# Optimization experiments

Measured on AMD Instinct MI355X. Metric: run time of the kernel, lower is better.

The kernel has to match this reference:

```python
import jax, jax.numpy as jnp
import numpy as np
import math

B, S, D_MODEL, H = 2, 2048, 1024, 16
D_HEAD = D_MODEL // H
THETA = 10000.0


def _init_linear(key, out_f, in_f):
    std = math.sqrt(2.0 / (out_f + in_f))
    w = jax.random.truncated_normal(key, -3.0, 3.0, (out_f, in_f), dtype=jnp.float32)
    return w * std


def setup_inputs() -> dict:
    key = jax.random.key(0)
    k1, k2, k3 = jax.random.split(key, 3)
    x = jax.random.normal(k1, (B, S, D_MODEL), dtype=jnp.float32)
    wqkv = _init_linear(k2, 3 * D_MODEL, D_MODEL)
    w_out = _init_linear(k3, D_MODEL, D_MODEL)
    # RoPE tables: positions [max_seq_len,1] * inv_freq [d_head//2]
    positions = jnp.arange(S, dtype=jnp.float32)[:, None]
    freqs = jnp.arange(0, D_HEAD, 2, dtype=jnp.float32) / D_HEAD
    inv_freq = 1.0 / (THETA ** freqs)
    angles = positions * inv_freq  # [S, D_HEAD//2]
    cos = jnp.cos(angles)
    sin = jnp.sin(angles)
    token_positions = jnp.arange(S, dtype=jnp.int32)
    return {"x": x, "wqkv": wqkv, "w_out": w_out, "cos": cos, "sin": sin,
            "token_positions": token_positions}


def _apply_rope(t, cos_pos, sin_pos):
    # t: [b, h, s, d], cos/sin_pos: [s, d//2] broadcast over b,h
    te = t[..., 0::2]
    to = t[..., 1::2]
    re = te * cos_pos - to * sin_pos
    ro = te * sin_pos + to * cos_pos
    # interleave even/odd back: [..., d//2, 2] -> [..., d]
    out = jnp.stack([re, ro], axis=-1)
    return out.reshape(t.shape)


def reference(x, wqkv, w_out, cos, sin, token_positions):
    b, s, d_model = x.shape
    qkv = jnp.einsum('oi,bsi->bso', wqkv, x)  # [b, s, 3*d_model]
    q, k, v = jnp.split(qkv, 3, axis=-1)

    def to_heads(t):
        return t.reshape(b, s, H, D_HEAD).transpose(0, 2, 1, 3)  # b h s d

    q, k, v = to_heads(q), to_heads(k), to_heads(v)

    cos_pos = cos[token_positions]  # [s, d_head//2]
    sin_pos = sin[token_positions]
    q = _apply_rope(q, cos_pos, sin_pos)
    k = _apply_rope(k, cos_pos, sin_pos)

    scores = jnp.einsum('bhqd,bhkd->bhqk', q, k) / math.sqrt(D_HEAD)
    causal = jnp.tril(jnp.ones((s, s), dtype=bool))  # ~triu(diag=1)
    scores = jnp.where(causal, scores, -jnp.inf)
    weights = jax.nn.softmax(scores, axis=-1)
    y = jnp.einsum('bhqk,bhkd->bhqd', weights, v)
    y = y.transpose(0, 2, 1, 3).reshape(b, s, d_model)
    return jnp.einsum('oi,bsi->bso', w_out, y)
```

## Files before the change

### kernel.cpp

```cpp
#include <hip/hip_runtime.h>
#include <hip/hip_bf16.h>


#define S_LEN 2048
#define DMODEL 1024
#define NH 16
#define QKVN 3072

typedef __attribute__((ext_vector_type(4))) short short4v;
typedef __attribute__((ext_vector_type(8))) short short8v;
typedef __attribute__((ext_vector_type(4))) float floatx4;

#define CSOFT 0.18033688f

__device__ __forceinline__ unsigned short f2bf(float f) {
  unsigned int u = __float_as_uint(f);
  u += 0x7FFFu + ((u >> 16) & 1u);
  return (unsigned short)(u >> 16);
}
__device__ __forceinline__ float bf2f(unsigned short u) {
  return __uint_as_float(((unsigned int)u) << 16);
}
__device__ __forceinline__ void gload16(const void* g, void* l) {
  __builtin_amdgcn_global_load_lds((const __attribute__((address_space(1))) void*)g,
                                   (__attribute__((address_space(3))) void*)l,
                                   16, 0, 0);
}

__global__ __launch_bounds__(256) void cast_bf16_perm_k(const float* __restrict__ in,
                                                        unsigned short* __restrict__ out,
                                                        int nchunk) {
  int i = blockIdx.x * 256 + threadIdx.x;
  if (i >= nchunk) return;
  int c = i & 3;
  const float4* f4 = reinterpret_cast<const float4*>(in);
  float4 lo = f4[(i >> 2) * 8 + c];
  float4 hi = f4[(i >> 2) * 8 + 4 + c];
  short8v o;
  o[0] = (short)f2bf(lo.x); o[1] = (short)f2bf(lo.y);
  o[2] = (short)f2bf(lo.z); o[3] = (short)f2bf(lo.w);
  o[4] = (short)f2bf(hi.x); o[5] = (short)f2bf(hi.y);
  o[6] = (short)f2bf(hi.z); o[7] = (short)f2bf(hi.w);
  reinterpret_cast<short8v*>(out)[i] = o;
}

template <bool OUT_BF16>
__global__ __launch_bounds__(256) void gemm_bt(const unsigned short* __restrict__ A,
                                               const unsigned short* __restrict__ Bm,
                                               void* __restrict__ Cp, int M, int N, int K) {
  __shared__ __align__(16) unsigned short As[128 * 32];
  __shared__ __align__(16) unsigned short Bs[128 * 32];
  const int tid = threadIdx.x;
  const int lane = tid & 63;
  const int w = tid >> 6;
  const int wm = w >> 1, wn = w & 1;
  const int l15 = lane & 15, l4 = lane >> 4;
  const int bm = blockIdx.y * 128, bn = blockIdx.x * 128;
  const int srow = lane >> 2;
  const int skc = (lane & 3) * 8;

  floatx4 acc[4][4] = {};

  for (int k0 = 0; k0 < K; k0 += 32) {
#pragma unroll
    for (int j = 0; j < 2; ++j) {
      const unsigned short* ga = A + (size_t)(bm + j * 64 + w * 16 + srow) * K + k0 + skc;
      gload16(ga, &As[j * 2048 + w * 512]);
      const unsigned short* gb = Bm + (size_t)(bn + j * 64 + w * 16 + srow) * K + k0 + skc;
      gload16(gb, &Bs[j * 2048 + w * 512]);
    }
    asm volatile("s_waitcnt vmcnt(0)" ::: "memory");
    __syncthreads();

    short8v af[4], bfr[4];
#pragma unroll
    for (int f = 0; f < 4; ++f) {
      af[f]  = *(const short8v*)(As + (wm * 64 + f * 16 + l15) * 32 + l4 * 8);
      bfr[f] = *(const short8v*)(Bs + (wn * 64 + f * 16 + l15) * 32 + l4 * 8);
    }
#pragma unroll
    for (int f = 0; f < 4; ++f)
#pragma unroll
      for (int g = 0; g < 4; ++g)
        acc[f][g] = __builtin_amdgcn_mfma_f32_16x16x32_bf16(af[f], bfr[g], acc[f][g], 0, 0, 0);
    __syncthreads();
  }

#pragma unroll
  for (int f = 0; f < 4; ++f)
#pragma unroll
    for (int g = 0; g < 4; ++g)
#pragma unroll
      for (int r = 0; r < 4; ++r) {
        int row = bm + wm * 64 + f * 16 + l4 * 4 + r;
        int col = bn + wn * 64 + g * 16 + l15;
        if (OUT_BF16)
          ((unsigned short*)Cp)[(size_t)row * N + col] = f2bf(acc[f][g][r]);
        else
          ((float*)Cp)[(size_t)row * N + col] = acc[f][g][r];
      }
}

__global__ __launch_bounds__(256) void rope_pack_k(const unsigned short* __restrict__ qkvb,
                                                   unsigned short* __restrict__ qp_,
                                                   unsigned short* __restrict__ kp_,
                                                   unsigned short* __restrict__ vtp_,
                                                   const float* __restrict__ cosp,
                                                   const float* __restrict__ sinp,
                                                   const int* __restrict__ tpos) {
  __shared__ unsigned short Vs[64][68];
  const int tid = threadIdx.x;
  const int bh = blockIdx.x >> 5;
  const int st = blockIdx.x & 31;
  const int b = bh >> 4, h = bh & 15;
  const int c = tid & 15, t0 = tid >> 4;
  const int s0 = st * 64;

#pragma unroll
  for (int it = 0; it < 4; ++it) {
    const int tl = it * 16 + t0;
    const int s = s0 + tl;
    const int tp = tpos[s];
    const size_t base = ((size_t)(b * S_LEN + s)) * QKVN + h * 64 + c * 4;
    const float co0 = cosp[tp * 32 + 2 * c], si0 = sinp[tp * 32 + 2 * c];
    const float co1 = cosp[tp * 32 + 2 * c + 1], si1 = sinp[tp * 32 + 2 * c + 1];
    {
      const float c0 = co0 * CSOFT, s0q = si0 * CSOFT;
      const float c1 = co1 * CSOFT, s1q = si1 * CSOFT;
      ushort4 rv = *(const ushort4*)(qkvb + base);
      float a0 = bf2f(rv.x), a1 = bf2f(rv.y), a2 = bf2f(rv.z), a3 = bf2f(rv.w);
      ushort4 ov;
      ov.x = f2bf(a0 * c0 - a1 * s0q); ov.y = f2bf(a0 * s0q + a1 * c0);
      ov.z = f2bf(a2 * c1 - a3 * s1q); ov.w = f2bf(a2 * s1q + a3 * c1);
      *(ushort4*)(qp_ + ((size_t)bh * S_LEN + s) * 64 + c * 4) = ov;
    }
    {
      ushort4 rv = *(const ushort4*)(qkvb + base + DMODEL);
      float a0 = bf2f(rv.x), a1 = bf2f(rv.y), a2 = bf2f(rv.z), a3 = bf2f(rv.w);
      ushort4 ov;
      ov.x = f2bf(a0 * co0 - a1 * si0); ov.y = f2bf(a0 * si0 + a1 * co0);
      ov.z = f2bf(a2 * co1 - a3 * si1); ov.w = f2bf(a2 * si1 + a3 * co1);
      *(ushort4*)(kp_ + ((size_t)bh * S_LEN + s) * 64 + c * 4) = ov;
    }
    {
      ushort4 rv = *(const ushort4*)(qkvb + base + 2 * DMODEL);
      *(ushort4*)(&Vs[tl][c * 4]) = rv;
    }
  }
  __syncthreads();
#pragma unroll
  for (int it = 0; it < 4; ++it) {
    const int d = it * 16 + t0;
    ushort4 ov;
    ov.x = Vs[c * 4 + 0][d]; ov.y = Vs[c * 4 + 1][d];
    ov.z = Vs[c * 4 + 2][d]; ov.w = Vs[c * 4 + 3][d];
    *(ushort4*)(vtp_ + ((size_t)bh * 64 + d) * S_LEN + s0 + c * 4) = ov;
  }
}

__device__ __forceinline__ short8v readfrag(const unsigned short* L, int row, int c2, int l4) {
  const int sw = row & 7;
  const int cl = c2 * 4 + (l4 >> 1);
  const int base = row * 64 + (l4 & 1) * 4;
  union { short4v h[2]; short8v v; } u;
  u.h[0] = *(const short4v*)(L + base + ((cl ^ sw) << 3));
  u.h[1] = *(const short4v*)(L + base + (((cl + 2) ^ sw) << 3));
  return u.v;
}

__device__ __forceinline__ void stage_tiles(const unsigned short* kg0, const unsigned short* vg0,
                                            int kt, unsigned short* Kb, unsigned short* Vb,
                                            int tid, int w) {
#pragma unroll
  for (int i = 0; i < 2; ++i) {
    int jj = i * 256 + tid;
    int row = jj >> 3;
    int cc = (jj & 7) ^ (row & 7);
    gload16(kg0 + (size_t)kt * 4096 + row * 64 + cc * 8, Kb + (i * 256 + w * 64) * 8);
    gload16(vg0 + (size_t)row * S_LEN + kt * 64 + cc * 8, Vb + (i * 256 + w * 64) * 8);
  }
}

__global__ __launch_bounds__(256) void attn_mfma(const unsigned short* __restrict__ qp_,
                                                 const unsigned short* __restrict__ kp_,
                                                 const unsigned short* __restrict__ vtp_,
                                                 unsigned short* __restrict__ yb) {
  __shared__ __align__(16) unsigned short Kl[2][4096];
  __shared__ __align__(16) unsigned short Vl[2][4096];
  const int tid = threadIdx.x;
  const int lane = tid & 63, w = tid >> 6;
  const int l15 = lane & 15, l4 = lane >> 4;
  const int j = blockIdx.x;
  const int bh = (j & 7) + 8 * (j >> 7);
  const int pair = (j >> 3) & 15;
  const int b = bh >> 4, h = bh & 15;

  const unsigned short* kg0 = kp_ + (size_t)bh * S_LEN * 64;
  const unsigned short* vg0 = vtp_ + (size_t)bh * 64 * S_LEN;

  for (int pass = 0; pass < 2; ++pass) {
    const int qt = pass ? pair : 31 - pair;
    const unsigned short* qp = qp_ + ((size_t)bh * S_LEN + qt * 64 + w * 16 + l15) * 64;
    short8v qf[2];
#pragma unroll
    for (int c2 = 0; c2 < 2; ++c2) {
      union { short4v h[2]; short8v v; } u;
      u.h[0] = *(const short4v*)(qp + c2 * 32 + 4 * l4);
      u.h[1] = *(const short4v*)(qp + c2 * 32 + 16 + 4 * l4);
      qf[c2] = u.v;
    }
    floatx4 o[4] = {};
    float mrun = -1e30f, lsum = 0.f;

    stage_tiles(kg0, vg0, 0, Kl[0], Vl[0], tid, w);

    for (int kt = 0; kt <= qt; ++kt) {
      const int cur = kt & 1;
      if (kt < qt) {
        stage_tiles(kg0, vg0, kt + 1, Kl[cur ^ 1], Vl[cur ^ 1], tid, w);
        asm volatile("s_waitcnt vmcnt(4)" ::: "memory");
      } else {
        asm volatile("s_waitcnt vmcnt(0)" ::: "memory");
      }
      __syncthreads();

      const unsigned short* Kc = Kl[cur];
      const unsigned short* Vc = Vl[cur];
      const bool diag = (kt == qt);
      float s_[4][4];
      __builtin_amdgcn_s_setprio(1);
#pragma unroll
      for (int g = 0; g < 4; ++g) {
        if (diag && g > w) {
          s_[g][0] = s_[g][1] = s_[g][2] = s_[g][3] = -INFINITY;
          continue;
        }
        short8v k0 = readfrag(Kc, g * 16 + l15, 0, l4);
        short8v k1 = readfrag(Kc, g * 16 + l15, 1, l4);
        floatx4 t = {0.f, 0.f, 0.f, 0.f};
        t = __builtin_amdgcn_mfma_f32_16x16x32_bf16(k0, qf[0], t, 0, 0, 0);
        t = __builtin_amdgcn_mfma_f32_16x16x32_bf16(k1, qf[1], t, 0, 0, 0);
#pragma unroll
        for (int r = 0; r < 4; ++r) {
          float v = t[r];
          if (diag && g == w && (l4 * 4 + r > l15)) v = -INFINITY;
          s_[g][r] = v;
        }
      }
      __builtin_amdgcn_s_setprio(0);

      float tm = -INFINITY;
#pragma unroll
      for (int g = 0; g < 4; ++g)
#pragma unroll
        for (int r = 0; r < 4; ++r) tm = fmaxf(tm, s_[g][r]);
      tm = fmaxf(tm, __shfl_xor(tm, 16));
      tm = fmaxf(tm, __shfl_xor(tm, 32));

      if (!__all(tm <= mrun + 3.0f)) {
        float nm = fmaxf(mrun, tm);
        float rs = exp2f(mrun - nm);
        mrun = nm;
        lsum *= rs;
        float rsr[4];
#pragma unroll
        for (int r = 0; r < 4; ++r) rsr[r] = __shfl(rs, l4 * 4 + r);
#pragma unroll
        for (int dt = 0; dt < 4; ++dt)
#pragma unroll
          for (int r = 0; r < 4; ++r) o[dt][r] *= rsr[r];
      }

      union { unsigned short u[16]; short8v v[2]; } pk;
      float psum = 0.f;
#pragma unroll
      for (int g = 0; g < 4; ++g)
#pragma unroll
        for (int r = 0; r < 4; ++r) {
          float p = exp2f(s_[g][r] - mrun);
          psum += p;
          pk.u[g * 4 + r] = f2bf(p);
        }
      lsum += psum;

      __builtin_amdgcn_s_setprio(1);
#pragma unroll
      for (int dt = 0; dt < 4; ++dt) {
        short8v v0 = readfrag(Vc, dt * 16 + l15, 0, l4);
        short8v v1 = readfrag(Vc, dt * 16 + l15, 1, l4);
        o[dt] = __builtin_amdgcn_mfma_f32_16x16x32_bf16(pk.v[0], v0, o[dt], 0, 0, 0);
        o[dt] = __builtin_amdgcn_mfma_f32_16x16x32_bf16(pk.v[1], v1, o[dt], 0, 0, 0);
      }
      __builtin_amdgcn_s_setprio(0);
      __syncthreads();
    }

    lsum += __shfl_xor(lsum, 16);
    lsum += __shfl_xor(lsum, 32);
    float linv = 1.f / lsum;
    float lr[4];
#pragma unroll
    for (int r = 0; r < 4; ++r) lr[r] = __shfl(linv, l4 * 4 + r);
#pragma unroll
    for (int dt = 0; dt < 4; ++dt)
#pragma unroll
      for (int r = 0; r < 4; ++r) {
        size_t row = (size_t)(b * S_LEN + qt * 64 + w * 16 + l4 * 4 + r);
        int col = (h * 2 + (dt >> 1)) * 32 + (l15 >> 2) * 8 + (l15 & 3) + 4 * (dt & 1);
        yb[row * DMODEL + col] = f2bf(o[dt][r] * lr[r]);
      }
  }
}

extern "C" void kernel_launch(void* const* d_in, const int* in_sizes, int n_in,
                              void* d_out, int out_size, void* d_ws, size_t ws_size,
                              hipStream_t stream) {
  const float* x     = (const float*)d_in[0];
  const float* wqkv  = (const float*)d_in[1];
  const float* w_out = (const float*)d_in[2];
  const float* cosp  = (const float*)d_in[3];
  const float* sinp  = (const float*)d_in[4];
  const int*   tpos  = (const int*)d_in[5];
  float* out = (float*)d_out;
  char* ws = (char*)d_ws;

  const size_t MB = 1024 * 1024;
  unsigned short* xb    = (unsigned short*)(ws + 0);
  unsigned short* wqkvb = (unsigned short*)(ws + 8 * MB);
  unsigned short* wob   = (unsigned short*)(ws + 14 * MB);
  unsigned short* qkvb  = (unsigned short*)(ws + 16 * MB);
  unsigned short* qpk   = (unsigned short*)(ws + 40 * MB);
  unsigned short* kpk   = (unsigned short*)(ws + 48 * MB);
  unsigned short* vtpk  = (unsigned short*)(ws + 56 * MB);
  unsigned short* yb    = (unsigned short*)(ws + 0);

  cast_bf16_perm_k<<<2048, 256, 0, stream>>>(x, xb, 524288);
  cast_bf16_perm_k<<<1536, 256, 0, stream>>>(wqkv, wqkvb, 393216);
  cast_bf16_perm_k<<<512, 256, 0, stream>>>(w_out, wob, 131072);

  gemm_bt<true><<<dim3(24, 32), 256, 0, stream>>>(xb, wqkvb, qkvb, 4096, QKVN, 1024);

  rope_pack_k<<<1024, 256, 0, stream>>>(qkvb, qpk, kpk, vtpk, cosp, sinp, tpos);

  attn_mfma<<<512, 256, 0, stream>>>(qpk, kpk, vtpk, yb);

  gemm_bt<false><<<dim3(8, 32), 256, 0, stream>>>(yb, wob, out, 4096, DMODEL, 1024);
}
```

Before: 221.8 us.

## Permute Q/K/V packing for 128-bit LDS reads, swizzle GEMM LDS, one q-tile per block

The rope pack kernel now writes Q, K and V^T with a permuted column order. This lets attention load each MFMA fragment with one 128-bit LDS read instead of two 64-bit reads, and load Q fragments directly. The GEMM rotates its 16-byte chunk placement in LDS to reduce bank conflicts. Attention no longer pairs a long and a short q-tile in one block: it launches 1024 blocks with one q-tile each, longest tiles first, which relies on the hardware scheduler to balance the causal work instead of the explicit pairing.

```diff
diff --git a/kernel.cpp b/kernel.cpp
--- a/kernel.cpp
+++ b/kernel.cpp
@@ -25,6 +25,9 @@
   __builtin_amdgcn_global_load_lds((const __attribute__((address_space(1))) void*)g,
                                    (__attribute__((address_space(3))) void*)l,
                                    16, 0, 0);
+}
+__device__ __forceinline__ int perm4(int c) {
+  return (c >> 3) * 32 + (c & 3) * 8 + ((c >> 2) & 1) * 4;
 }
 
 __global__ __launch_bounds__(256) void cast_bf16_perm_k(const float* __restrict__ in,
@@ -57,16 +60,17 @@
   const int l15 = lane & 15, l4 = lane >> 4;
   const int bm = blockIdx.y * 128, bn = blockIdx.x * 128;
   const int srow = lane >> 2;
-  const int skc = (lane & 3) * 8;
+  const int schunk = ((lane & 3) - ((lane >> 3) & 3)) & 3;
+  const int rslot = (l4 + (l15 >> 1)) & 3;
 
   floatx4 acc[4][4] = {};
 
   for (int k0 = 0; k0 < K; k0 += 32) {
 #pragma unroll
     for (int j = 0; j < 2; ++j) {
-      const unsigned short* ga = A + (size_t)(bm + j * 64 + w * 16 + srow) * K + k0 + skc;
+      const unsigned short* ga = A + (size_t)(bm + j * 64 + w * 16 + srow) * K + k0 + schunk * 8;
       gload16(ga, &As[j * 2048 + w * 512]);
-      const unsigned short* gb = Bm + (size_t)(bn + j * 64 + w * 16 + srow) * K + k0 + skc;
+      const unsigned short* gb = Bm + (size_t)(bn + j * 64 + w * 16 + srow) * K + k0 + schunk * 8;
       gload16(gb, &Bs[j * 2048 + w * 512]);
     }
     asm volatile("s_waitcnt vmcnt(0)" ::: "memory");
@@ -75,8 +79,8 @@
     short8v af[4], bfr[4];
 #pragma unroll
     for (int f = 0; f < 4; ++f) {
-      af[f]  = *(const short8v*)(As + (wm * 64 + f * 16 + l15) * 32 + l4 * 8);
-      bfr[f] = *(const short8v*)(Bs + (wn * 64 + f * 16 + l15) * 32 + l4 * 8);
+      af[f]  = *(const short8v*)(As + (wm * 64 + f * 16 + l15) * 32 + rslot * 8);
+      bfr[f] = *(const short8v*)(Bs + (wn * 64 + f * 16 + l15) * 32 + rslot * 8);
     }
 #pragma unroll
     for (int f = 0; f < 4; ++f)
@@ -115,6 +119,7 @@
   const int b = bh >> 4, h = bh & 15;
   const int c = tid & 15, t0 = tid >> 4;
   const int s0 = st * 64;
+  const int pc = perm4(c);
 
 #pragma unroll
   for (int it = 0; it < 4; ++it) {
@@ -132,7 +137,7 @@
       ushort4 ov;
       ov.x = f2bf(a0 * c0 - a1 * s0q); ov.y = f2bf(a0 * s0q + a1 * c0);
       ov.z = f2bf(a2 * c1 - a3 * s1q); ov.w = f2bf(a2 * s1q + a3 * c1);
-      *(ushort4*)(qp_ + ((size_t)bh * S_LEN + s) * 64 + c * 4) = ov;
+      *(ushort4*)(qp_ + ((size_t)bh * S_LEN + s) * 64 + pc) = ov;
     }
     {
       ushort4 rv = *(const ushort4*)(qkvb + base + DMODEL);
@@ -140,7 +145,7 @@
       ushort4 ov;
       ov.x = f2bf(a0 * co0 - a1 * si0); ov.y = f2bf(a0 * si0 + a1 * co0);
       ov.z = f2bf(a2 * co1 - a3 * si1); ov.w = f2bf(a2 * si1 + a3 * co1);
-      *(ushort4*)(kp_ + ((size_t)bh * S_LEN + s) * 64 + c * 4) = ov;
+      *(ushort4*)(kp_ + ((size_t)bh * S_LEN + s) * 64 + pc) = ov;
     }
     {
       ushort4 rv = *(const ushort4*)(qkvb + base + 2 * DMODEL);
@@ -154,18 +159,12 @@
     ushort4 ov;
     ov.x = Vs[c * 4 + 0][d]; ov.y = Vs[c * 4 + 1][d];
     ov.z = Vs[c * 4 + 2][d]; ov.w = Vs[c * 4 + 3][d];
-    *(ushort4*)(vtp_ + ((size_t)bh * 64 + d) * S_LEN + s0 + c * 4) = ov;
-  }
-}
-
-__device__ __forceinline__ short8v readfrag(const unsigned short* L, int row, int c2, int l4) {
-  const int sw = row & 7;
-  const int cl = c2 * 4 + (l4 >> 1);
-  const int base = row * 64 + (l4 & 1) * 4;
-  union { short4v h[2]; short8v v; } u;
-  u.h[0] = *(const short4v*)(L + base + ((cl ^ sw) << 3));
-  u.h[1] = *(const short4v*)(L + base + (((cl + 2) ^ sw) << 3));
-  return u.v;
+    *(ushort4*)(vtp_ + ((size_t)bh * 64 + d) * S_LEN + s0 + pc) = ov;
+  }
+}
+
+__device__ __forceinline__ short8v readfrag128(const unsigned short* L, int row, int cc) {
+  return *(const short8v*)(L + row * 64 + (((cc) ^ (row & 7)) << 3));
 }
 
 __device__ __forceinline__ void stage_tiles(const unsigned short* kg0, const unsigned short* vg0,
@@ -191,125 +190,119 @@
   const int lane = tid & 63, w = tid >> 6;
   const int l15 = lane & 15, l4 = lane >> 4;
   const int j = blockIdx.x;
-  const int bh = (j & 7) + 8 * (j >> 7);
-  const int pair = (j >> 3) & 15;
+  const int bh = (j & 7) + 8 * ((j >> 3) & 3);
+  const int qt = 31 - (j >> 5);
   const int b = bh >> 4, h = bh & 15;
 
   const unsigned short* kg0 = kp_ + (size_t)bh * S_LEN * 64;
   const unsigned short* vg0 = vtp_ + (size_t)bh * 64 * S_LEN;
 
-  for (int pass = 0; pass < 2; ++pass) {
-    const int qt = pass ? pair : 31 - pair;
-    const unsigned short* qp = qp_ + ((size_t)bh * S_LEN + qt * 64 + w * 16 + l15) * 64;
-    short8v qf[2];
-#pragma unroll
-    for (int c2 = 0; c2 < 2; ++c2) {
-      union { short4v h[2]; short8v v; } u;
-      u.h[0] = *(const short4v*)(qp + c2 * 32 + 4 * l4);
-      u.h[1] = *(const short4v*)(qp + c2 * 32 + 16 + 4 * l4);
-      qf[c2] = u.v;
-    }
-    floatx4 o[4] = {};
-    float mrun = -1e30f, lsum = 0.f;
-
-    stage_tiles(kg0, vg0, 0, Kl[0], Vl[0], tid, w);
-
-    for (int kt = 0; kt <= qt; ++kt) {
-      const int cur = kt & 1;
-      if (kt < qt) {
-        stage_tiles(kg0, vg0, kt + 1, Kl[cur ^ 1], Vl[cur ^ 1], tid, w);
-        asm volatile("s_waitcnt vmcnt(4)" ::: "memory");
-      } else {
-        asm volatile("s_waitcnt vmcnt(0)" ::: "memory");
+  const unsigned short* qp = qp_ + ((size_t)bh * S_LEN + qt * 64 + w * 16 + l15) * 64;
+  short8v qf[2];
+#pragma unroll
+  for (int c2 = 0; c2 < 2; ++c2)
+    qf[c2] = *(const short8v*)(qp + c2 * 32 + l4 * 8);
+
+  floatx4 o[4] = {};
+  float mrun = -1e30f, lsum = 0.f;
+
+  stage_tiles(kg0, vg0, 0, Kl[0], Vl[0], tid, w);
+
+  for (int kt = 0; kt <= qt; ++kt) {
+    const int cur = kt & 1;
+    if (kt < qt) {
+      stage_tiles(kg0, vg0, kt + 1, Kl[cur ^ 1], Vl[cur ^ 1], tid, w);
+      asm volatile("s_waitcnt vmcnt(4)" ::: "memory");
+    } else {
+      asm volatile("s_waitcnt vmcnt(0)" ::: "memory");
+    }
+    __syncthreads();
+
+    const unsigned short* Kc = Kl[cur];
+    const unsigned short* Vc = Vl[cur];
+    const bool diag = (kt == qt);
+    float s_[4][4];
+    __builtin_amdgcn_s_setprio(1);
+#pragma unroll
+    for (int g = 0; g < 4; ++g) {
+      if (diag && g > w) {
+        s_[g][0] = s_[g][1] = s_[g][2] = s_[g][3] = -INFINITY;
+        continue;
       }
-      __syncthreads();
-
-      const unsigned short* Kc = Kl[cur];
-      const unsigned short* Vc = Vl[cur];
-      const bool diag = (kt == qt);
-      float s_[4][4];
-      __builtin_amdgcn_s_setprio(1);
-#pragma unroll
-      for (int g = 0; g < 4; ++g) {
-        if (diag && g > w) {
-          s_[g][0] = s_[g][1] = s_[g][2] = s_[g][3] = -INFINITY;
-          continue;
-        }
-        short8v k0 = readfrag(Kc, g * 16 + l15, 0, l4);
-        short8v k1 = readfrag(Kc, g * 16 + l15, 1, l4);
-        floatx4 t = {0.f, 0.f, 0.f, 0.f};
-        t = __builtin_amdgcn_mfma_f32_16x16x32_bf16(k0, qf[0], t, 0, 0, 0);
-        t = __builtin_amdgcn_mfma_f32_16x16x32_bf16(k1, qf[1], t, 0, 0, 0);
-#pragma unroll
-        for (int r = 0; r < 4; ++r) {
-          float v = t[r];
-          if (diag && g == w && (l4 * 4 + r > l15)) v = -INFINITY;
-          s_[g][r] = v;
-        }
+      short8v k0 = readfrag128(Kc, g * 16 + l15, l4);
+      short8v k1 = readfrag128(Kc, g * 16 + l15, 4 + l4);
+      floatx4 t = {0.f, 0.f, 0.f, 0.f};
+      t = __builtin_amdgcn_mfma_f32_16x16x32_bf16(k0, qf[0], t, 0, 0, 0);
+      t = __builtin_amdgcn_mfma_f32_16x16x32_bf16(k1, qf[1], t, 0, 0, 0);
+#pragma unroll
+      for (int r = 0; r < 4; ++r) {
+        float v = t[r];
+        if (diag && g == w && (l4 * 4 + r > l15)) v = -INFINITY;
+        s_[g][r] = v;
       }
-      __builtin_amdgcn_s_setprio(0);
-
-      float tm = -INFINITY;
-#pragma unroll
-      for (int g = 0; g < 4; ++g)
-#pragma unroll
-        for (int r = 0; r < 4; ++r) tm = fmaxf(tm, s_[g][r]);
-      tm = fmaxf(tm, __shfl_xor(tm, 16));
-      tm = fmaxf(tm, __shfl_xor(tm, 32));
-
-      if (!__all(tm <= mrun + 3.0f)) {
-        float nm = fmaxf(mrun, tm);
-        float rs = exp2f(mrun - nm);
-        mrun = nm;
-        lsum *= rs;
-        float rsr[4];
-#pragma unroll
-        for (int r = 0; r < 4; ++r) rsr[r] = __shfl(rs, l4 * 4 + r);
-#pragma unroll
-        for (int dt = 0; dt < 4; ++dt)
-#pragma unroll
-          for (int r = 0; r < 4; ++r) o[dt][r] *= rsr[r];
+    }
+    __builtin_amdgcn_s_setprio(0);
+
+    float tm = -INFINITY;
+#pragma unroll
+    for (int g = 0; g < 4; ++g)
+#pragma unroll
+      for (int r = 0; r < 4; ++r) tm = fmaxf(tm, s_[g][r]);
+    tm = fmaxf(tm, __shfl_xor(tm, 16));
+    tm = fmaxf(tm, __shfl_xor(tm, 32));
+
+    if (!__all(tm <= mrun + 3.0f)) {
+      float nm = fmaxf(mrun, tm);
+      float rs = exp2f(mrun - nm);
+      mrun = nm;
+      lsum *= rs;
+      float rsr[4];
+#pragma unroll
+      for (int r = 0; r < 4; ++r) rsr[r] = __shfl(rs, l4 * 4 + r);
+#pragma unroll
+      for (int dt = 0; dt < 4; ++dt)
+#pragma unroll
+        for (int r = 0; r < 4; ++r) o[dt][r] *= rsr[r];
+    }
+
+    union { unsigned short u[16]; short8v v[2]; } pk;
+    float psum = 0.f;
+#pragma unroll
+    for (int g = 0; g < 4; ++g)
+#pragma unroll
+      for (int r = 0; r < 4; ++r) {
+        float p = exp2f(s_[g][r] - mrun);
+        psum += p;
+        pk.u[g * 4 + r] = f2bf(p);
       }
-
-      union { unsigned short u[16]; short8v v[2]; } pk;
-      float psum = 0.f;
-#pragma unroll
-      for (int g = 0; g < 4; ++g)
-#pragma unroll
-        for (int r = 0; r < 4; ++r) {
-          float p = exp2f(s_[g][r] - mrun);
-          psum += p;
-          pk.u[g * 4 + r] = f2bf(p);
-        }
-      lsum += psum;
-
-      __builtin_amdgcn_s_setprio(1);
-#pragma unroll
-      for (int dt = 0; dt < 4; ++dt) {
-        short8v v0 = readfrag(Vc, dt * 16 + l15, 0, l4);
-        short8v v1 = readfrag(Vc, dt * 16 + l15, 1, l4);
-        o[dt] = __builtin_amdgcn_mfma_f32_16x16x32_bf16(pk.v[0], v0, o[dt], 0, 0, 0);
-        o[dt] = __builtin_amdgcn_mfma_f32_16x16x32_bf16(pk.v[1], v1, o[dt], 0, 0, 0);
-      }
-      __builtin_amdgcn_s_setprio(0);
-      __syncthreads();
-    }
-
-    lsum += __shfl_xor(lsum, 16);
-    lsum += __shfl_xor(lsum, 32);
-    float linv = 1.f / lsum;
-    float lr[4];
-#pragma unroll
-    for (int r = 0; r < 4; ++r) lr[r] = __shfl(linv, l4 * 4 + r);
-#pragma unroll
-    for (int dt = 0; dt < 4; ++dt)
-#pragma unroll
-      for (int r = 0; r < 4; ++r) {
-        size_t row = (size_t)(b * S_LEN + qt * 64 + w * 16 + l4 * 4 + r);
-        int col = (h * 2 + (dt >> 1)) * 32 + (l15 >> 2) * 8 + (l15 & 3) + 4 * (dt & 1);
-        yb[row * DMODEL + col] = f2bf(o[dt][r] * lr[r]);
-      }
-  }
+    lsum += psum;
+
+    __builtin_amdgcn_s_setprio(1);
+#pragma unroll
+    for (int dt = 0; dt < 4; ++dt) {
+      short8v v0 = readfrag128(Vc, dt * 16 + l15, l4);
+      short8v v1 = readfrag128(Vc, dt * 16 + l15, 4 + l4);
+      o[dt] = __builtin_amdgcn_mfma_f32_16x16x32_bf16(pk.v[0], v0, o[dt], 0, 0, 0);
+      o[dt] = __builtin_amdgcn_mfma_f32_16x16x32_bf16(pk.v[1], v1, o[dt], 0, 0, 0);
+    }
+    __builtin_amdgcn_s_setprio(0);
+    __syncthreads();
+  }
+
+  lsum += __shfl_xor(lsum, 16);
+  lsum += __shfl_xor(lsum, 32);
+  float linv = 1.f / lsum;
+  float lr[4];
+#pragma unroll
+  for (int r = 0; r < 4; ++r) lr[r] = __shfl(linv, l4 * 4 + r);
+#pragma unroll
+  for (int dt = 0; dt < 4; ++dt)
+#pragma unroll
+    for (int r = 0; r < 4; ++r) {
+      size_t row = (size_t)(b * S_LEN + qt * 64 + w * 16 + l4 * 4 + r);
+      int col = (h * 2 + (dt >> 1)) * 32 + (l15 >> 2) * 8 + (l15 & 3) + 4 * (dt & 1);
+      yb[row * DMODEL + col] = f2bf(o[dt][r] * lr[r]);
+    }
 }
 
 extern "C" void kernel_launch(void* const* d_in, const int* in_sizes, int n_in,
@@ -342,7 +335,7 @@
 
   rope_pack_k<<<1024, 256, 0, stream>>>(qkvb, qpk, kpk, vtpk, cosp, sinp, tpos);
 
-  attn_mfma<<<512, 256, 0, stream>>>(qpk, kpk, vtpk, yb);
+  attn_mfma<<<1024, 256, 0, stream>>>(qpk, kpk, vtpk, yb);
 
   gemm_bt<false><<<dim3(8, 32), 256, 0, stream>>>(yb, wob, out, 4096, DMODEL, 1024);
 }
```

After: 205.6 us. 7.3% less time.
